# Kernel tuning notes

Measured on AMD Instinct MI355X. Metric: run time of the kernel, lower is better.

## Reference

```python
import jax, jax.numpy as jnp
import numpy as np

N, E, G = 30000, 240000, 1500
EMB, NODE_DIM, EDGE_DIM, TASKS = 300, 9, 3, 12
L_ENC, L_RAT = 5, 2
GAMMA, T_CON = 0.4, 0.2


def _w(key, shape, fan_in):
    return jax.random.normal(key, shape, jnp.float32) / np.float32(np.sqrt(fan_in))


def setup_inputs() -> dict:
    key = jax.random.key(0)
    ks = jax.random.split(key, 32)
    inp = {}
    inp['x'] = jax.random.normal(ks[0], (N, NODE_DIM), jnp.float32)
    inp['edge_attr'] = jax.random.normal(ks[1], (E, EDGE_DIM), jnp.float32)
    inp['edge_index'] = jax.random.randint(ks[2], (2, E), 0, N, jnp.int32)
    b = jnp.sort(jax.random.randint(ks[3], (N,), 0, G, jnp.int32))
    inp['batch'] = b.at[0].set(0).at[-1].set(G - 1)
    u = jax.random.uniform(ks[4], (N, 2), jnp.float32, 1e-6, 1.0 - 1e-6)
    inp['gumbel'] = -jnp.log(-jnp.log(u))  # standard Gumbel noise (tau=1)
    inp['perm'] = jax.random.permutation(ks[5], G).astype(jnp.int32)
    inp['W_enc'] = _w(ks[6], (NODE_DIM, EMB), NODE_DIM)
    inp['b_enc'] = jnp.zeros((EMB,), jnp.float32)
    inp['We_g'] = _w(ks[7], (L_ENC, EDGE_DIM, EMB), EDGE_DIM)
    inp['be_g'] = jnp.zeros((L_ENC, EMB), jnp.float32)
    inp['W1_g'] = _w(ks[8], (L_ENC, EMB, 2 * EMB), EMB)
    inp['b1_g'] = jnp.zeros((L_ENC, 2 * EMB), jnp.float32)
    inp['W2_g'] = _w(ks[9], (L_ENC, 2 * EMB, EMB), 2 * EMB)
    inp['b2_g'] = jnp.zeros((L_ENC, EMB), jnp.float32)
    inp['We_r'] = _w(ks[10], (L_RAT, EDGE_DIM, EMB), EDGE_DIM)
    inp['be_r'] = jnp.zeros((L_RAT, EMB), jnp.float32)
    inp['W1_r'] = _w(ks[11], (L_RAT, EMB, 2 * EMB), EMB)
    inp['b1_r'] = jnp.zeros((L_RAT, 2 * EMB), jnp.float32)
    inp['W2_r'] = _w(ks[12], (L_RAT, 2 * EMB, EMB), 2 * EMB)
    inp['b2_r'] = jnp.zeros((L_RAT, EMB), jnp.float32)
    inp['Wg1'] = _w(ks[13], (EMB, 2 * EMB), EMB)
    inp['bg1'] = jnp.zeros((2 * EMB,), jnp.float32)
    inp['Wg2'] = _w(ks[14], (2 * EMB, 2), 2 * EMB)
    inp['bg2'] = jnp.zeros((2,), jnp.float32)
    inp['Wp1'] = _w(ks[15], (EMB, 2 * EMB), EMB)
    inp['bp1'] = jnp.zeros((2 * EMB,), jnp.float32)
    inp['Wp2'] = _w(ks[16], (2 * EMB, TASKS), 2 * EMB)
    inp['bp2'] = jnp.zeros((TASKS,), jnp.float32)
    return inp


def _gin_stack(x, src, dst, edge_attr, We, be, W1, b1, W2, b2):
    # GIN-style message passing with edge features, residual, JK='last'.
    L = We.shape[0]
    for l in range(L):
        e = edge_attr @ We[l] + be[l]                               # [E, EMB]
        msg = jax.nn.relu(x[src] + e)                                # gather [E, EMB]
        agg = jax.ops.segment_sum(msg, dst, num_segments=x.shape[0])  # scatter [N, EMB]
        h = jax.nn.relu((agg + x) @ W1[l] + b1[l]) @ W2[l] + b2[l]
        if l < L - 1:
            h = jax.nn.relu(h)
        x = x + h  # residual
    return x


def _mlp2(h, Wa, ba, Wb, bb):
    # Linear -> (BN=identity in eval) -> ReLU -> (Dropout=identity) -> Linear
    return jax.nn.relu(h @ Wa + ba) @ Wb + bb


def _forward(x, edge_attr, gumbel, W_enc, b_enc, We_g, be_g, W1_g, b1_g, W2_g, b2_g,
             We_r, be_r, W1_r, b1_r, W2_r, b2_r, Wg1, bg1, Wg2, bg2, Wp1, bp1, Wp2, bp2,
             edge_index, batch, perm):
    src, dst = edge_index[0], edge_index[1]
    cnt = jnp.clip(jax.ops.segment_sum(jnp.ones((x.shape[0],), jnp.float32), batch, num_segments=G), 1.0)[:, None]

    def gmean(v):
        return jax.ops.segment_sum(v, batch, num_segments=G) / cnt

    x_feat = x @ W_enc + b_enc                                      # node encoder
    h_node = _gin_stack(x_feat, src, dst, edge_attr, We_g, be_g, W1_g, b1_g, W2_g, b2_g)
    x_rat = _gin_stack(x_feat, src, dst, edge_attr, We_r, be_r, W1_r, b1_r, W2_r, b2_r)

    gate_logits = _mlp2(x_rat, Wg1, bg1, Wg2, bg2)                  # [N, 2]
    gate = jax.nn.softmax(gate_logits + gumbel, axis=-1)[:, 1:2]     # gumbel-softmax (soft), keep last col

    h_r = gmean(gate * h_node)
    h_env = gmean((1.0 - gate) * h_node)
    r_num = jax.ops.segment_sum(gate, batch, num_segments=G) + 1e-8
    env_num = jax.ops.segment_sum(1.0 - gate, batch, num_segments=G) + 1e-8

    pred_rem = _mlp2(h_r, Wp1, bp1, Wp2, bp2)
    loss_reg = jnp.abs(r_num / (r_num + env_num) - GAMMA).mean()

    h_out = gmean(h_node)
    na = jnp.linalg.norm(h_r, axis=1)
    nb = jnp.linalg.norm(h_out, axis=1)
    nc = jnp.linalg.norm(h_env, axis=1)
    sim = jnp.exp((h_r @ h_out.T) / (na[:, None] * nb[None, :] + 1e-8) / T_CON)
    sim_cp = jnp.exp((h_r @ h_env.T) / (na[:, None] * nc[None, :] + 1e-8) / T_CON)
    pos = jnp.diagonal(sim)
    loss_con = -jnp.log(pos / (sim_cp.sum(axis=1) + pos)).mean()

    pred_rep = _mlp2(h_r + h_env[perm], Wp1, bp1, Wp2, bp2)
    return pred_rep, pred_rem, loss_reg, loss_con


def reference(x, edge_attr, gumbel, W_enc, b_enc, We_g, be_g, W1_g, b1_g, W2_g, b2_g,
              We_r, be_r, W1_r, b1_r, W2_r, b2_r, Wg1, bg1, Wg2, bg2, Wp1, bp1, Wp2, bp2,
              edge_index, batch, perm):
    return _forward(x, edge_attr, gumbel, W_enc, b_enc, We_g, be_g, W1_g, b1_g, W2_g, b2_g,
                    We_r, be_r, W1_r, b1_r, W2_r, b2_r, Wg1, bg1, Wg2, bg2, Wp1, bp1, Wp2, bp2,
                    edge_index, batch, perm)
```

## Files before the change

### kernel.cpp

```cpp
#include <hip/hip_runtime.h>
#include <hip/hip_bf16.h>

typedef __hip_bfloat16 bf16;
typedef __attribute__((ext_vector_type(8))) short bf16x8;
typedef __attribute__((ext_vector_type(4))) float f32x4;

#define NN 30000
#define NE 240000
#define NG 1500
#define EMB 300
#define HID 600
#define NTASK 12
#define SEM 320
#define SHID 608
#define CG 75
#define NBLK_SCAN 118

__device__ __forceinline__ float tof(bf16 v){ return __bfloat162float(v); }
__device__ __forceinline__ bf16  tob(float v){ return __float2bfloat16(v); }
__device__ __forceinline__ float b2f(unsigned short u){ return __uint_as_float(((unsigned)u)<<16); }

__global__ __launch_bounds__(256) void k_zero_i(int* __restrict__ p, int n){
    int i = blockIdx.x*256 + threadIdx.x;
    if (i < n) p[i] = 0;
// ... 40 lines not shown
    for (int off=1; off<256; off<<=1){
        int add = (t>=off) ? s[t-off] : 0;
        __syncthreads();
        s[t] += add;
        __syncthreads();
    }
    int excl = s[t] - v + boff[b];
    if (i < NN){ indptr[i] = excl; cursor[i] = excl; }
    if (i == 0) indptr[NN] = NE;
}

__global__ __launch_bounds__(256) void k_scatter(const int* __restrict__ dst, int* __restrict__ cursor,
                                                 int* __restrict__ eid){
    int e = blockIdx.x*256 + threadIdx.x;
    if (e < NE){ int p = atomicAdd(&cursor[dst[e]], 1); eid[p] = e; }
}

__global__ __launch_bounds__(256) void k_eprep(const int* __restrict__ eid, const int* __restrict__ src,
                                               const float* __restrict__ eattr, float4* __restrict__ epack){
    int k = blockIdx.x*256 + threadIdx.x;
    if (k >= NE) return;
    int e = eid[k];
    float4 p;
    p.x = __int_as_float(src[e]);
    p.y = eattr[e*3]; p.z = eattr[e*3+1]; p.w = eattr[e*3+2];
    epack[k] = p;
}

__global__ __launch_bounds__(256) void k_gstart(const int* __restrict__ batch, int* __restrict__ gstart){
    int g = blockIdx.x*256 + threadIdx.x;
    if (g > NG) return;
    if (g == NG){ gstart[NG] = NN; return; }
    int lo=0, hi=NN;
    while (lo<hi){ int mid=(lo+hi)>>1; if (batch[mid] < g) lo=mid+1; else hi=mid; }
    gstart[g] = lo;
}

__global__ __launch_bounds__(256) void k_wprep(const float* __restrict__ W, bf16* __restrict__ Wt,
                                               int K, int Kp, int N){
    __shared__ float t[32][33];
    const float* Wz = W + (size_t)blockIdx.z*K*N;
    bf16* Wtz = Wt + (size_t)blockIdx.z*N*Kp;
    int n0 = blockIdx.x*32, k0 = blockIdx.y*32;
    int tx = threadIdx.x & 31, ty = threadIdx.x >> 5;
    #pragma unroll
    for (int i=0;i<4;i++){
        int k = k0 + ty + i*8, n = n0 + tx;
        t[ty+i*8][tx] = (k<K && n<N) ? Wz[(size_t)k*N+n] : 0.f;
    }
    __syncthreads();
    #pragma unroll
    for (int i=0;i<4;i++){
        int n = n0 + ty + i*8, k = k0 + tx;
        if (n<N && k<Kp) Wtz[(size_t)n*Kp+k] = tob(t[tx][ty+i*8]);
    }
}

__global__ __launch_bounds__(256) void k_encoder(const float* __restrict__ x, const float* __restrict__ W,
                                                 const float* __restrict__ b, bf16* __restrict__ xfeat){
    int idx = blockIdx.x*256 + threadIdx.x;
    if (idx >= NN*EMB) return;
    int n = idx / EMB, c = idx - n*EMB;
    float acc = b[c];
    #pragma unroll
    for (int k=0;k<9;k++) acc += x[n*9+k] * W[k*EMB+c];
    xfeat[(size_t)n*SEM + c] = tob(acc);
}

__global__ __launch_bounds__(256) void k_agg4(const bf16* __restrict__ cur, const float* __restrict__ We,
                      const float* __restrict__ be, const float4* __restrict__ epack,
                      const int* __restrict__ indptr, bf16* __restrict__ apx){
    int idx = blockIdx.x*256 + threadIdx.x;
    if (idx >= NN*CG) return;
    int n = idx / CG, cg = idx - n*CG;
    int c0 = cg*4;
    float w0[4], w1[4], w2[4], bbv[4], acc[4];
    #pragma unroll
    for (int j=0;j<4;j++){
        w0[j] = We[c0+j]; w1[j] = We[EMB+c0+j]; w2[j] = We[2*EMB+c0+j]; bbv[j] = be[c0+j];
    }
    ushort4 hs = *(const ushort4*)&cur[(size_t)n*SEM + c0];
    acc[0]=b2f(hs.x); acc[1]=b2f(hs.y); acc[2]=b2f(hs.z); acc[3]=b2f(hs.w);
    int k  = indptr[n], k1 = indptr[n+1];
    for (; k+4 <= k1; k += 4){
        float4 e0 = epack[k], e1 = epack[k+1], e2 = epack[k+2], e3 = epack[k+3];
        int s0 = __float_as_int(e0.x), s1 = __float_as_int(e1.x);
        int s2 = __float_as_int(e2.x), s3 = __float_as_int(e3.x);
        ushort4 ha = *(const ushort4*)&cur[(size_t)s0*SEM + c0];
        ushort4 hb = *(const ushort4*)&cur[(size_t)s1*SEM + c0];
        ushort4 hc = *(const ushort4*)&cur[(size_t)s2*SEM + c0];
        ushort4 hd = *(const ushort4*)&cur[(size_t)s3*SEM + c0];
        float fa[4] = {b2f(ha.x), b2f(ha.y), b2f(ha.z), b2f(ha.w)};
        float fb[4] = {b2f(hb.x), b2f(hb.y), b2f(hb.z), b2f(hb.w)};
        float fc[4] = {b2f(hc.x), b2f(hc.y), b2f(hc.z), b2f(hc.w)};
        float fd[4] = {b2f(hd.x), b2f(hd.y), b2f(hd.z), b2f(hd.w)};
        #pragma unroll
        for (int j=0;j<4;j++){
            float va = fa[j] + e0.y*w0[j] + e0.z*w1[j] + e0.w*w2[j] + bbv[j];
            float vb = fb[j] + e1.y*w0[j] + e1.z*w1[j] + e1.w*w2[j] + bbv[j];
            float vc = fc[j] + e2.y*w0[j] + e2.z*w1[j] + e2.w*w2[j] + bbv[j];
            float vd = fd[j] + e3.y*w0[j] + e3.z*w1[j] + e3.w*w2[j] + bbv[j];
            acc[j] += fmaxf(va, 0.f) + fmaxf(vb, 0.f) + fmaxf(vc, 0.f) + fmaxf(vd, 0.f);
        }
    }
    for (; k+2 <= k1; k += 2){
        float4 e0 = epack[k], e1 = epack[k+1];
        int s0 = __float_as_int(e0.x), s1 = __float_as_int(e1.x);
        ushort4 ha = *(const ushort4*)&cur[(size_t)s0*SEM + c0];
        ushort4 hb = *(const ushort4*)&cur[(size_t)s1*SEM + c0];
        float fa[4] = {b2f(ha.x), b2f(ha.y), b2f(ha.z), b2f(ha.w)};
        float fb[4] = {b2f(hb.x), b2f(hb.y), b2f(hb.z), b2f(hb.w)};
        #pragma unroll
        for (int j=0;j<4;j++){
            float va = fa[j] + e0.y*w0[j] + e0.z*w1[j] + e0.w*w2[j] + bbv[j];
            float vb = fb[j] + e1.y*w0[j] + e1.z*w1[j] + e1.w*w2[j] + bbv[j];
            acc[j] += fmaxf(va, 0.f) + fmaxf(vb, 0.f);
        }
    }
    if (k < k1){
        float4 e0 = epack[k];
        int s0 = __float_as_int(e0.x);
        ushort4 ha = *(const ushort4*)&cur[(size_t)s0*SEM + c0];
        float fa[4] = {b2f(ha.x), b2f(ha.y), b2f(ha.z), b2f(ha.w)};
        #pragma unroll
        for (int j=0;j<4;j++){
            float va = fa[j] + e0.y*w0[j] + e0.z*w1[j] + e0.w*w2[j] + bbv[j];
            acc[j] += fmaxf(va, 0.f);
        }
    }
    ushort4 o;
    o.x = __bfloat16_as_ushort(tob(acc[0]));
    o.y = __bfloat16_as_ushort(tob(acc[1]));
    o.z = __bfloat16_as_ushort(tob(acc[2]));
    o.w = __bfloat16_as_ushort(tob(acc[3]));
    *(ushort4*)&apx[(size_t)n*SEM + c0] = o;
}

__global__ __launch_bounds__(256) void k_gemm2(const bf16* __restrict__ A, const bf16* __restrict__ Bt,
        const float* __restrict__ bias, const bf16* __restrict__ R, bf16* __restrict__ C,
        int M, int N, int Kp, int ldc, int relu_out){
    __shared__ __align__(16) char ldsbuf[34816];
    short (*Asl)[64][8] = reinterpret_cast<short(*)[64][8]>(ldsbuf);
    short (*Bsl)[64][8] = reinterpret_cast<short(*)[64][8]>(ldsbuf + 8192);
    short* Ct = reinterpret_cast<short*>(ldsbuf);
    const int CS = 136;
    int tid = threadIdx.x;
    int wave = tid >> 6, lane = tid & 63;
    int wm = wave >> 1, wn = wave & 1;
    int m0 = blockIdx.y*128, n0 = blockIdx.x*128;

    int srow = tid >> 1;
    int sq   = (tid & 1) * 2;
    int grA = min(m0 + srow, M-1);
    int grB = min(n0 + srow, N-1);
    const bf16* pA = A  + (size_t)grA*Kp + sq*8;
    const bf16* pB = Bt + (size_t)grB*Kp + sq*8;
    short* ldsA0 = &Asl[srow>>4][ sq   *16 + (srow&15)][0];
    short* ldsA1 = &Asl[srow>>4][(sq+1)*16 + (srow&15)][0];
    short* ldsB0 = &Bsl[srow>>4][ sq   *16 + (srow&15)][0];
    short* ldsB1 = &Bsl[srow>>4][(sq+1)*16 + (srow&15)][0];

    f32x4 acc[4][4];
    #pragma unroll
    for (int i=0;i<4;i++){
        #pragma unroll
        for (int j=0;j<4;j++) acc[i][j] = (f32x4){0.f,0.f,0.f,0.f};
    }

    int KC = Kp >> 5;
    uint4 ra0 = *(const uint4*)(pA);
    uint4 ra1 = *(const uint4*)(pA + 8);
    uint4 rb0 = *(const uint4*)(pB);
    uint4 rb1 = *(const uint4*)(pB + 8);

    for (int kc=0; kc<KC; ++kc){
        *(uint4*)ldsA0 = ra0; *(uint4*)ldsA1 = ra1;
        *(uint4*)ldsB0 = rb0; *(uint4*)ldsB1 = rb1;
        __syncthreads();
        if (kc+1 < KC){
            const bf16* qA = pA + (kc+1)*32;
            const bf16* qB = pB + (kc+1)*32;
            ra0 = *(const uint4*)(qA); ra1 = *(const uint4*)(qA+8);
            rb0 = *(const uint4*)(qB); rb1 = *(const uint4*)(qB+8);
        }
        bf16x8 af[4], bfr[4];
        #pragma unroll
        for (int i=0;i<4;i++) af[i]  = *(const bf16x8*)&Asl[wm*4+i][lane][0];
        #pragma unroll
        for (int j=0;j<4;j++) bfr[j] = *(const bf16x8*)&Bsl[wn*4+j][lane][0];
        #pragma unroll
        for (int i=0;i<4;i++){
            #pragma unroll
            for (int j=0;j<4;j++)
                acc[i][j] = __builtin_amdgcn_mfma_f32_16x16x32_bf16(af[i], bfr[j], acc[i][j], 0, 0, 0);
        }
        __syncthreads();
    }

    int lq = lane >> 4, lr = lane & 15;
    #pragma unroll
    for (int i=0;i<4;i++){
        int rl = (wm*4+i)*16 + lq*4;
        #pragma unroll
        for (int j=0;j<4;j++){
            int cl = (wn*4+j)*16 + lr;
            float bv = bias[min(n0+cl, N-1)];
            #pragma unroll
            for (int r=0;r<4;r++){
                float v = acc[i][j][r] + bv;
                if (relu_out) v = fmaxf(v, 0.f);
                Ct[(rl+r)*CS + cl] = (short)__bfloat16_as_ushort(tob(v));
            }
        }
    }
    __syncthreads();
    #pragma unroll
    for (int p=0;p<8;p++){
        int rl = p*16 + (tid>>4);
        int cl = (tid&15)*8;
        int row = m0 + rl, col = n0 + cl;
        if (row < M && col < N){
            union { short s8[8]; uint4 v; } u;
            u.v = *(uint4*)&Ct[rl*CS + cl];
            if (R){
                const bf16* rp = &R[(size_t)row*ldc + col];
                #pragma unroll
                for (int e=0;e<8;e++){
                    float v = b2f((unsigned short)u.s8[e]) + tof(rp[e]);
                    u.s8[e] = (short)__bfloat16_as_ushort(tob(v));
                }
            }
            *(uint4*)&C[(size_t)row*ldc + col] = u.v;
        }
    }
}

__device__ __forceinline__ void stage_tile(const short* __restrict__ P, int RB, int K, int r0, int k0,
                                           short (*lds)[64][8], int tid){
    #pragma unroll
    for (int s=0;s<2;s++){
        int seg = tid*2+s;
        int row = seg>>2, q = seg&3;
        int gr = r0 + row;
        int gk = k0 + q*8;
        union { short s8[8]; uint4 v; } u;
        if (gr < RB && gk + 8 <= K){
            const uint2* p = (const uint2*)(P + (size_t)gr*K + gk);
            uint2 lo = p[0], hi = p[1];
            u.v.x = lo.x; u.v.y = lo.y; u.v.z = hi.x; u.v.w = hi.y;
        } else {
            #pragma unroll
            for (int j=0;j<8;j++){
                int kk = gk + j;
                u.s8[j] = (gr < RB && kk < K) ? P[(size_t)gr*K + kk] : (short)0;
            }
        }
        *(uint4*)&lds[row>>4][q*16 + (row&15)][0] = u.v;
    }
}

__global__ __launch_bounds__(256) void k_sim_mfma(const bf16* __restrict__ A, const bf16* __restrict__ Bt,
                      const float* __restrict__ na, const float* __restrict__ nc, float* __restrict__ C){
    __shared__ __align__(16) short Asl[8][64][8];
    __shared__ __align__(16) short Bsl[8][64][8];
    int tid = threadIdx.x;
    int wave = tid >> 6, lane = tid & 63;
    int wm = wave >> 1, wn = wave & 1;
    int m0 = blockIdx.y*128, n0 = blockIdx.x*128;
    f32x4 acc[4][4];
    #pragma unroll
    for (int i=0;i<4;i++){
        #pragma unroll
        for (int j=0;j<4;j++) acc[i][j] = (f32x4){0.f,0.f,0.f,0.f};
    }
    for (int k0=0; k0<SEM; k0+=32){
        stage_tile((const short*)A,  NG, SEM, m0, k0, Asl, tid);
        stage_tile((const short*)Bt, NG, SEM, n0, k0, Bsl, tid);
        __syncthreads();
        bf16x8 af[4], bfr[4];
        #pragma unroll
        for (int i=0;i<4;i++) af[i]  = *(const bf16x8*)&Asl[wm*4+i][lane][0];
        #pragma unroll
        for (int j=0;j<4;j++) bfr[j] = *(const bf16x8*)&Bsl[wn*4+j][lane][0];
        #pragma unroll
        for (int i=0;i<4;i++){
            #pragma unroll
            for (int j=0;j<4;j++)
                acc[i][j] = __builtin_amdgcn_mfma_f32_16x16x32_bf16(af[i], bfr[j], acc[i][j], 0, 0, 0);
        }
        __syncthreads();
    }
    int lq = lane >> 4, lr = lane & 15;
    #pragma unroll
    for (int i=0;i<4;i++){
        int rb = m0 + (wm*4+i)*16 + lq*4;
        #pragma unroll
        for (int j=0;j<4;j++){
            int col = n0 + (wn*4+j)*16 + lr;
            if (col >= NG) continue;
            float ncj = nc[col];
            #pragma unroll
            for (int r=0;r<4;r++){
                int row = rb + r;
                if (row >= NG) continue;
                C[(size_t)row*NG+col] = expf(acc[i][j][r] * 5.0f / (na[row]*ncj + 1e-8f));
            }
        }
    }
}

__global__ __launch_bounds__(256) void k_gate(const bf16* __restrict__ mid, const float* __restrict__ Wg2,
                      const float* __restrict__ bg2, const float* __restrict__ gumbel, float* __restrict__ gate){
    int gw = blockIdx.x*4 + (threadIdx.x >> 6);
    int lane = threadIdx.x & 63;
    if (gw >= NN) return;
    float s0=0.f, s1=0.f;
// ... 112 lines not shown
    #pragma unroll
    for (int t=0;t<NTASK;t++) acc[t] = 0.f;
    for (int i=lane;i<HID;i+=64){
        float h = tof(hidP[(size_t)r*SHID+i]);
        const float4* wp = (const float4*)&Wp2[i*NTASK];
        float4 wa = wp[0], wb = wp[1], wc = wp[2];
        acc[0]+=h*wa.x; acc[1]+=h*wa.y; acc[2]+=h*wa.z; acc[3]+=h*wa.w;
        acc[4]+=h*wb.x; acc[5]+=h*wb.y; acc[6]+=h*wb.z; acc[7]+=h*wb.w;
        acc[8]+=h*wc.x; acc[9]+=h*wc.y; acc[10]+=h*wc.z; acc[11]+=h*wc.w;
    }
    #pragma unroll
    for (int t=0;t<NTASK;t++){
        for (int off=32; off>0; off>>=1) acc[t] += __shfl_down(acc[t], off);
    }
    if (lane==0){
        float* dst = (r < NG) ? &out[NG*NTASK + r*NTASK] : &out[(r-NG)*NTASK];
        #pragma unroll
        for (int t=0;t<NTASK;t++) dst[t] = acc[t] + bp2[t];
    }
}

__global__ __launch_bounds__(256) void k_loss(const float* __restrict__ cntf, const float* __restrict__ rnum,
                      const float* __restrict__ pos, const float* __restrict__ S, float* __restrict__ out){
    __shared__ float ra[256], rb[256];
    int t = threadIdx.x;
    float a=0.f, b=0.f;
    for (int g=t; g<NG; g+=256){
        float r = rnum[g] + 1e-8f;
        float e = (cntf[g] - rnum[g]) + 1e-8f;
        a += fabsf(r/(r+e) - 0.4f);
        float p = pos[g];
        b += -logf(p/(S[g]+p));
    }
    ra[t]=a; rb[t]=b; __syncthreads();
    for (int off=128; off>0; off>>=1){ if (t<off){ ra[t]+=ra[t+off]; rb[t]+=rb[t+off]; } __syncthreads(); }
    if (t==0){
        out[2*NG*NTASK]   = ra[0]/NG;
        out[2*NG*NTASK+1] = rb[0]/NG;
    }
}

extern "C" void kernel_launch(void* const* d_in, const int* in_sizes, int n_in,
                              void* d_out, int out_size, void* d_ws, size_t ws_size,
                              hipStream_t stream) {
    const float* x      = (const float*)d_in[0];
    const float* eattr  = (const float*)d_in[1];
    const int*   eidx   = (const int*)d_in[2];
    const int*   batch  = (const int*)d_in[3];
    const float* gumbel = (const float*)d_in[4];
    const int*   perm   = (const int*)d_in[5];
    const float* W_enc  = (const float*)d_in[6];
    const float* b_enc  = (const float*)d_in[7];
    const float* We_g   = (const float*)d_in[8];
    const float* be_g   = (const float*)d_in[9];
    const float* W1_g   = (const float*)d_in[10];
    const float* b1_g   = (const float*)d_in[11];
    const float* W2_g   = (const float*)d_in[12];
    const float* b2_g   = (const float*)d_in[13];
    const float* We_r   = (const float*)d_in[14];
    const float* be_r   = (const float*)d_in[15];
    const float* W1_r   = (const float*)d_in[16];
    const float* b1_r   = (const float*)d_in[17];
    const float* W2_r   = (const float*)d_in[18];
    const float* b2_r   = (const float*)d_in[19];
    const float* Wg1    = (const float*)d_in[20];
    const float* bg1    = (const float*)d_in[21];
    const float* Wg2    = (const float*)d_in[22];
    const float* bg2    = (const float*)d_in[23];
    const float* Wp1    = (const float*)d_in[24];
    const float* bp1    = (const float*)d_in[25];
    const float* Wp2    = (const float*)d_in[26];
    const float* bp2    = (const float*)d_in[27];
    float* out = (float*)d_out;

    const int* srcArr = eidx;
    const int* dstArr = eidx + NE;

    char* w = (char*)d_ws;
    size_t off = 0;
    auto alloc = [&](size_t bytes)->char*{ char* p = w + off; off += (bytes + 255) & ~(size_t)255; return p; };
    bf16* xfeat = (bf16*)alloc((size_t)NN*SEM*2);
    bf16* cur   = (bf16*)alloc((size_t)NN*SEM*2);
    bf16* apx   = (bf16*)alloc((size_t)NN*SEM*2);
    char* midc  = alloc((size_t)NN*SHID*2);
    bf16* mid   = (bf16*)midc;
    float* simcp = (float*)midc;
    bf16* Pbuf   = (bf16*)(midc + 12*1024*1024);
    bf16* hidP   = (bf16*)(midc + 20*1024*1024);
    bf16* wt1g  = (bf16*)alloc((size_t)5*HID*SEM*2);
    bf16* wt2g  = (bf16*)alloc((size_t)5*EMB*SHID*2);
    bf16* wt1r  = (bf16*)alloc((size_t)2*HID*SEM*2);
    bf16* wt2r  = (bf16*)alloc((size_t)2*EMB*SHID*2);
    bf16* wtg1  = (bf16*)alloc((size_t)HID*SEM*2);
    bf16* wtp1  = (bf16*)alloc((size_t)HID*SEM*2);
    float4* epack = (float4*)alloc((size_t)NE*16);
    float* gate  = (float*)alloc((size_t)NN*4);
    float* sumh  = (float*)alloc((size_t)NG*EMB*4);
    float* sumgh = (float*)alloc((size_t)NG*EMB*4);
    float* hr    = (float*)alloc((size_t)NG*EMB*4);
    float* henv  = (float*)alloc((size_t)NG*EMB*4);
    float* hout  = (float*)alloc((size_t)NG*EMB*4);
    bf16* hrb    = (bf16*)alloc((size_t)NG*SEM*2);
    bf16* henvb  = (bf16*)alloc((size_t)NG*SEM*2);
    float* rnum  = (float*)alloc(NG*4);
    float* cntf  = (float*)alloc(NG*4);
    float* na    = (float*)alloc(NG*4);
    float* ncv   = (float*)alloc(NG*4);
    float* pos   = (float*)alloc(NG*4);
    float* Ssum  = (float*)alloc(NG*4);
    int* deg     = (int*)alloc((size_t)NN*4);
    int* indptr  = (int*)alloc((size_t)(NN+1)*4);
    int* cursor  = (int*)alloc((size_t)NN*4);
    int* eid     = (int*)alloc((size_t)NE*4);
    int* gstart  = (int*)alloc((size_t)(NG+1)*4);
    int* bsum    = (int*)alloc((size_t)NBLK_SCAN*4);
    int* boff    = (int*)alloc((size_t)NBLK_SCAN*4);

    const int NB_NE  = (NE+255)/256;
    const int NB_NC  = (NN*EMB+255)/256;
    const int NB_AG  = (NN*CG+255)/256;
    const int NB_GP  = (NG*SEM+255)/256;

    k_zero_i <<<(NN+255)/256, 256, 0, stream>>>(deg, NN);
    k_hist   <<<NB_NE, 256, 0, stream>>>(dstArr, deg);
    k_scanA  <<<NBLK_SCAN, 256, 0, stream>>>(deg, bsum);
    k_scanB  <<<1, 128, 0, stream>>>(bsum, boff);
    k_scanC  <<<NBLK_SCAN, 256, 0, stream>>>(deg, boff, indptr, cursor);
    k_scatter<<<NB_NE, 256, 0, stream>>>(dstArr, cursor, eid);
    k_eprep  <<<NB_NE, 256, 0, stream>>>(eid, srcArr, eattr, epack);
    k_gstart <<<(NG+256)/256, 256, 0, stream>>>(batch, gstart);

    {
        dim3 g1t((HID+31)/32, SEM/32, 5);
        dim3 g2t((EMB+31)/32, SHID/32, 5);
        k_wprep<<<g1t, 256, 0, stream>>>(W1_g, wt1g, EMB, SEM, HID);
        k_wprep<<<g2t, 256, 0, stream>>>(W2_g, wt2g, HID, SHID, EMB);
        dim3 g1t2((HID+31)/32, SEM/32, 2);
        dim3 g2t2((EMB+31)/32, SHID/32, 2);
        k_wprep<<<g1t2, 256, 0, stream>>>(W1_r, wt1r, EMB, SEM, HID);
        k_wprep<<<g2t2, 256, 0, stream>>>(W2_r, wt2r, HID, SHID, EMB);
        dim3 g1t1((HID+31)/32, SEM/32, 1);
        k_wprep<<<g1t1, 256, 0, stream>>>(Wg1, wtg1, EMB, SEM, HID);
        k_wprep<<<g1t1, 256, 0, stream>>>(Wp1, wtp1, EMB, SEM, HID);
    }

    dim3 gm1((HID+127)/128, (NN+127)/128);
    dim3 gm2((EMB+127)/128, (NN+127)/128);

    k_encoder<<<NB_NC, 256, 0, stream>>>(x, W_enc, b_enc, xfeat);

    for (int l=0; l<2; l++){
        const bf16* in = (l==0) ? xfeat : cur;
        k_agg4 <<<NB_AG, 256, 0, stream>>>(in, We_r + l*3*EMB, be_r + l*EMB, epack, indptr, apx);
        k_gemm2<<<gm1, 256, 0, stream>>>(apx, wt1r + (size_t)l*HID*SEM, b1_r + l*HID, nullptr, mid,
                                         NN, HID, SEM, SHID, 1);
        k_gemm2<<<gm2, 256, 0, stream>>>(mid, wt2r + (size_t)l*EMB*SHID, b2_r + l*EMB, in, cur,
                                         NN, EMB, SHID, SEM, (l<1)?1:0);
    }
    k_gemm2<<<gm1, 256, 0, stream>>>(cur, wtg1, bg1, nullptr, mid, NN, HID, SEM, SHID, 1);
    k_gate<<<NN/4, 256, 0, stream>>>(mid, Wg2, bg2, gumbel, gate);

    for (int l=0; l<5; l++){
        const bf16* in = (l==0) ? xfeat : cur;
        k_agg4 <<<NB_AG, 256, 0, stream>>>(in, We_g + l*3*EMB, be_g + l*EMB, epack, indptr, apx);
        k_gemm2<<<gm1, 256, 0, stream>>>(apx, wt1g + (size_t)l*HID*SEM, b1_g + l*HID, nullptr, mid,
                                         NN, HID, SEM, SHID, 1);
        k_gemm2<<<gm2, 256, 0, stream>>>(mid, wt2g + (size_t)l*EMB*SHID, b2_g + l*EMB, in, cur,
                                         NN, EMB, SHID, SEM, (l<4)?1:0);
    }

    k_pool  <<<NG, 320, 0, stream>>>(cur, gate, gstart, sumh, sumgh);
    k_rnum  <<<(NG+3)/4, 256, 0, stream>>>(gate, gstart, rnum, cntf);
    k_mean  <<<NB_GP, 256, 0, stream>>>(sumh, sumgh, cntf, hr, henv, hout, hrb, henvb);
    k_pbuild<<<NB_GP, 256, 0, stream>>>(hr, henv, perm, Pbuf);
    k_norm  <<<(NG+3)/4, 256, 0, stream>>>(hr, henv, hout, na, ncv, pos);
    dim3 gsim((NG+127)/128, (NG+127)/128);
    k_sim_mfma<<<gsim, 256, 0, stream>>>(hrb, henvb, na, ncv, simcp);
    k_rowsum<<<NG, 256, 0, stream>>>(simcp, Ssum);
    dim3 gph((HID+127)/128, (2*NG+127)/128);
    k_gemm2<<<gph, 256, 0, stream>>>(Pbuf, wtp1, bp1, nullptr, hidP, 2*NG, HID, SEM, SHID, 1);
    k_pred  <<<(2*NG+3)/4, 256, 0, stream>>>(hidP, Wp2, bp2, out);
    k_loss  <<<1, 256, 0, stream>>>(cntf, rnum, pos, Ssum, out);
}
```

Before: 996.6 us.

## Widen GEMM tiles to 128x256 and software-pipeline gather loads in aggregation

```diff
diff --git a/kernel.cpp b/kernel.cpp
--- a/kernel.cpp
+++ b/kernel.cpp
@@ -146,14 +146,9 @@
     ushort4 hs = *(const ushort4*)&cur[(size_t)n*SEM + c0];
     acc[0]=b2f(hs.x); acc[1]=b2f(hs.y); acc[2]=b2f(hs.z); acc[3]=b2f(hs.w);
     int k  = indptr[n], k1 = indptr[n+1];
-    for (; k+4 <= k1; k += 4){
-        float4 e0 = epack[k], e1 = epack[k+1], e2 = epack[k+2], e3 = epack[k+3];
-        int s0 = __float_as_int(e0.x), s1 = __float_as_int(e1.x);
-        int s2 = __float_as_int(e2.x), s3 = __float_as_int(e3.x);
-        ushort4 ha = *(const ushort4*)&cur[(size_t)s0*SEM + c0];
-        ushort4 hb = *(const ushort4*)&cur[(size_t)s1*SEM + c0];
-        ushort4 hc = *(const ushort4*)&cur[(size_t)s2*SEM + c0];
-        ushort4 hd = *(const ushort4*)&cur[(size_t)s3*SEM + c0];
+
+    auto accum4 = [&](float4 e0, float4 e1, float4 e2, float4 e3,
+                      ushort4 ha, ushort4 hb, ushort4 hc, ushort4 hd){
         float fa[4] = {b2f(ha.x), b2f(ha.y), b2f(ha.z), b2f(ha.w)};
         float fb[4] = {b2f(hb.x), b2f(hb.y), b2f(hb.z), b2f(hb.w)};
         float fc[4] = {b2f(hc.x), b2f(hc.y), b2f(hc.z), b2f(hc.w)};
@@ -166,22 +161,29 @@
             float vd = fd[j] + e3.y*w0[j] + e3.z*w1[j] + e3.w*w2[j] + bbv[j];
             acc[j] += fmaxf(va, 0.f) + fmaxf(vb, 0.f) + fmaxf(vc, 0.f) + fmaxf(vd, 0.f);
         }
-    }
-    for (; k+2 <= k1; k += 2){
-        float4 e0 = epack[k], e1 = epack[k+1];
-        int s0 = __float_as_int(e0.x), s1 = __float_as_int(e1.x);
-        ushort4 ha = *(const ushort4*)&cur[(size_t)s0*SEM + c0];
-        ushort4 hb = *(const ushort4*)&cur[(size_t)s1*SEM + c0];
-        float fa[4] = {b2f(ha.x), b2f(ha.y), b2f(ha.z), b2f(ha.w)};
-        float fb[4] = {b2f(hb.x), b2f(hb.y), b2f(hb.z), b2f(hb.w)};
-        #pragma unroll
-        for (int j=0;j<4;j++){
-            float va = fa[j] + e0.y*w0[j] + e0.z*w1[j] + e0.w*w2[j] + bbv[j];
-            float vb = fb[j] + e1.y*w0[j] + e1.z*w1[j] + e1.w*w2[j] + bbv[j];
-            acc[j] += fmaxf(va, 0.f) + fmaxf(vb, 0.f);
-        }
-    }
-    if (k < k1){
+    };
+
+    if (k + 4 <= k1){
+        float4 e0 = epack[k], e1 = epack[k+1], e2 = epack[k+2], e3 = epack[k+3];
+        ushort4 h0 = *(const ushort4*)&cur[(size_t)__float_as_int(e0.x)*SEM + c0];
+        ushort4 h1 = *(const ushort4*)&cur[(size_t)__float_as_int(e1.x)*SEM + c0];
+        ushort4 h2 = *(const ushort4*)&cur[(size_t)__float_as_int(e2.x)*SEM + c0];
+        ushort4 h3 = *(const ushort4*)&cur[(size_t)__float_as_int(e3.x)*SEM + c0];
+        while (k + 8 <= k1){
+            float4 f0 = epack[k+4], f1 = epack[k+5], f2 = epack[k+6], f3 = epack[k+7];
+            ushort4 g0 = *(const ushort4*)&cur[(size_t)__float_as_int(f0.x)*SEM + c0];
+            ushort4 g1 = *(const ushort4*)&cur[(size_t)__float_as_int(f1.x)*SEM + c0];
+            ushort4 g2 = *(const ushort4*)&cur[(size_t)__float_as_int(f2.x)*SEM + c0];
+            ushort4 g3 = *(const ushort4*)&cur[(size_t)__float_as_int(f3.x)*SEM + c0];
+            accum4(e0,e1,e2,e3, h0,h1,h2,h3);
+            e0=f0; e1=f1; e2=f2; e3=f3;
+            h0=g0; h1=g1; h2=g2; h3=g3;
+            k += 4;
+        }
+        accum4(e0,e1,e2,e3, h0,h1,h2,h3);
+        k += 4;
+    }
+    for (; k < k1; k++){
         float4 e0 = epack[k];
         int s0 = __float_as_int(e0.x);
         ushort4 ha = *(const ushort4*)&cur[(size_t)s0*SEM + c0];
@@ -200,9 +202,13 @@
     *(ushort4*)&apx[(size_t)n*SEM + c0] = o;
 }
 
-__global__ __launch_bounds__(256) void k_gemm2(const bf16* __restrict__ A, const bf16* __restrict__ Bt,
+template<int NF>
+__global__ __launch_bounds__(256) void k_gemmT(const bf16* __restrict__ A, const bf16* __restrict__ Bt,
         const float* __restrict__ bias, const bf16* __restrict__ R, bf16* __restrict__ C,
         int M, int N, int Kp, int ldc, int relu_out){
+    constexpr int TN = NF*32;
+    constexpr int SB = (TN*4)/256;
+    constexpr int PASSES = NF/4;
     __shared__ __align__(16) char ldsbuf[34816];
     short (*Asl)[64][8] = reinterpret_cast<short(*)[64][8]>(ldsbuf);
     short (*Bsl)[64][8] = reinterpret_cast<short(*)[64][8]>(ldsbuf + 8192);
@@ -211,51 +217,56 @@
     int tid = threadIdx.x;
     int wave = tid >> 6, lane = tid & 63;
     int wm = wave >> 1, wn = wave & 1;
-    int m0 = blockIdx.y*128, n0 = blockIdx.x*128;
-
-    int srow = tid >> 1;
-    int sq   = (tid & 1) * 2;
-    int grA = min(m0 + srow, M-1);
-    int grB = min(n0 + srow, N-1);
-    const bf16* pA = A  + (size_t)grA*Kp + sq*8;
-    const bf16* pB = Bt + (size_t)grB*Kp + sq*8;
-    short* ldsA0 = &Asl[srow>>4][ sq   *16 + (srow&15)][0];
-    short* ldsA1 = &Asl[srow>>4][(sq+1)*16 + (srow&15)][0];
-    short* ldsB0 = &Bsl[srow>>4][ sq   *16 + (srow&15)][0];
-    short* ldsB1 = &Bsl[srow>>4][(sq+1)*16 + (srow&15)][0];
-
-    f32x4 acc[4][4];
+    int m0 = blockIdx.y*128, n0 = blockIdx.x*TN;
+
+    int arow = tid >> 1, aq = (tid & 1)*2;
+    int grA = min(m0 + arow, M-1);
+    const bf16* pA = A + (size_t)grA*Kp + aq*8;
+    short* ldsA0 = &Asl[arow>>4][ aq   *16 + (arow&15)][0];
+    short* ldsA1 = &Asl[arow>>4][(aq+1)*16 + (arow&15)][0];
+    const bf16* pB[SB]; short* ldsB[SB];
+    #pragma unroll
+    for (int s=0;s<SB;s++){
+        int g = tid*SB + s; int br = g >> 2, bq = g & 3;
+        int grB = min(n0 + br, N-1);
+        pB[s] = Bt + (size_t)grB*Kp + bq*8;
+        ldsB[s] = &Bsl[br>>4][bq*16 + (br&15)][0];
+    }
+
+    f32x4 acc[4][NF];
     #pragma unroll
     for (int i=0;i<4;i++){
         #pragma unroll
-        for (int j=0;j<4;j++) acc[i][j] = (f32x4){0.f,0.f,0.f,0.f};
+        for (int j=0;j<NF;j++) acc[i][j] = (f32x4){0.f,0.f,0.f,0.f};
     }
 
     int KC = Kp >> 5;
-    uint4 ra0 = *(const uint4*)(pA);
+    uint4 ra0 = *(const uint4*)pA;
     uint4 ra1 = *(const uint4*)(pA + 8);
-    uint4 rb0 = *(const uint4*)(pB);
-    uint4 rb1 = *(const uint4*)(pB + 8);
+    uint4 rb[SB];
+    #pragma unroll
+    for (int s=0;s<SB;s++) rb[s] = *(const uint4*)pB[s];
 
     for (int kc=0; kc<KC; ++kc){
         *(uint4*)ldsA0 = ra0; *(uint4*)ldsA1 = ra1;
-        *(uint4*)ldsB0 = rb0; *(uint4*)ldsB1 = rb1;
+        #pragma unroll
+        for (int s=0;s<SB;s++) *(uint4*)ldsB[s] = rb[s];
         __syncthreads();
         if (kc+1 < KC){
             const bf16* qA = pA + (kc+1)*32;
-            const bf16* qB = pB + (kc+1)*32;
             ra0 = *(const uint4*)(qA); ra1 = *(const uint4*)(qA+8);
-            rb0 = *(const uint4*)(qB); rb1 = *(const uint4*)(qB+8);
-        }
-        bf16x8 af[4], bfr[4];
+            #pragma unroll
+            for (int s=0;s<SB;s++) rb[s] = *(const uint4*)(pB[s] + (kc+1)*32);
+        }
+        bf16x8 af[4], bfr[NF];
         #pragma unroll
         for (int i=0;i<4;i++) af[i]  = *(const bf16x8*)&Asl[wm*4+i][lane][0];
         #pragma unroll
-        for (int j=0;j<4;j++) bfr[j] = *(const bf16x8*)&Bsl[wn*4+j][lane][0];
+        for (int j=0;j<NF;j++) bfr[j] = *(const bf16x8*)&Bsl[wn*NF+j][lane][0];
         #pragma unroll
         for (int i=0;i<4;i++){
             #pragma unroll
-            for (int j=0;j<4;j++)
+            for (int j=0;j<NF;j++)
                 acc[i][j] = __builtin_amdgcn_mfma_f32_16x16x32_bf16(af[i], bfr[j], acc[i][j], 0, 0, 0);
         }
         __syncthreads();
@@ -263,39 +274,47 @@
 
     int lq = lane >> 4, lr = lane & 15;
     #pragma unroll
-    for (int i=0;i<4;i++){
-        int rl = (wm*4+i)*16 + lq*4;
-        #pragma unroll
-        for (int j=0;j<4;j++){
-            int cl = (wn*4+j)*16 + lr;
-            float bv = bias[min(n0+cl, N-1)];
+    for (int h=0; h<PASSES; h++){
+        if (PASSES == 1 || wn == h){
             #pragma unroll
-            for (int r=0;r<4;r++){
-                float v = acc[i][j][r] + bv;
-                if (relu_out) v = fmaxf(v, 0.f);
-                Ct[(rl+r)*CS + cl] = (short)__bfloat16_as_ushort(tob(v));
-            }
-        }
-    }
-    __syncthreads();
-    #pragma unroll
-    for (int p=0;p<8;p++){
-        int rl = p*16 + (tid>>4);
-        int cl = (tid&15)*8;
-        int row = m0 + rl, col = n0 + cl;
-        if (row < M && col < N){
-            union { short s8[8]; uint4 v; } u;
-            u.v = *(uint4*)&Ct[rl*CS + cl];
-            if (R){
-                const bf16* rp = &R[(size_t)row*ldc + col];
+            for (int i=0;i<4;i++){
+                int rl = (wm*4+i)*16 + lq*4;
                 #pragma unroll
-                for (int e=0;e<8;e++){
-                    float v = b2f((unsigned short)u.s8[e]) + tof(rp[e]);
-                    u.s8[e] = (short)__bfloat16_as_ushort(tob(v));
+                for (int j=0;j<NF;j++){
+                    int fl = (PASSES==1) ? (wn*4+j) : j;
+                    int cl = fl*16 + lr;
+                    int gcol = n0 + h*128 + cl;
+                    float bv = bias[min(gcol, N-1)];
+                    #pragma unroll
+                    for (int r=0;r<4;r++){
+                        float v = acc[i][j][r] + bv;
+                        if (relu_out) v = fmaxf(v, 0.f);
+                        Ct[(rl+r)*CS + cl] = (short)__bfloat16_as_ushort(tob(v));
+                    }
                 }
             }
-            *(uint4*)&C[(size_t)row*ldc + col] = u.v;
-        }
+        }
+        __syncthreads();
+        #pragma unroll
+        for (int p=0;p<8;p++){
+            int rl = p*16 + (tid>>4);
+            int cl = (tid&15)*8;
+            int row = m0 + rl, col = n0 + h*128 + cl;
+            if (row < M && col < N){
+                union { short s8[8]; uint4 v; } u;
+                u.v = *(uint4*)&Ct[rl*CS + cl];
+                if (R){
+                    const bf16* rp = &R[(size_t)row*ldc + col];
+                    #pragma unroll
+                    for (int e=0;e<8;e++){
+                        float v = b2f((unsigned short)u.s8[e]) + tof(rp[e]);
+                        u.s8[e] = (short)__bfloat16_as_ushort(tob(v));
+                    }
+                }
+                *(uint4*)&C[(size_t)row*ldc + col] = u.v;
+            }
+        }
+        if (h+1 < PASSES) __syncthreads();
     }
 }
 
@@ -636,29 +655,29 @@
         k_wprep<<<g1t1, 256, 0, stream>>>(Wp1, wtp1, EMB, SEM, HID);
     }
 
-    dim3 gm1((HID+127)/128, (NN+127)/128);
-    dim3 gm2((EMB+127)/128, (NN+127)/128);
+    dim3 gm1((HID+255)/256, (NN+127)/128);
+    dim3 gm2((EMB+255)/256, (NN+127)/128);
 
     k_encoder<<<NB_NC, 256, 0, stream>>>(x, W_enc, b_enc, xfeat);
 
     for (int l=0; l<2; l++){
         const bf16* in = (l==0) ? xfeat : cur;
         k_agg4 <<<NB_AG, 256, 0, stream>>>(in, We_r + l*3*EMB, be_r + l*EMB, epack, indptr, apx);
-        k_gemm2<<<gm1, 256, 0, stream>>>(apx, wt1r + (size_t)l*HID*SEM, b1_r + l*HID, nullptr, mid,
-                                         NN, HID, SEM, SHID, 1);
-        k_gemm2<<<gm2, 256, 0, stream>>>(mid, wt2r + (size_t)l*EMB*SHID, b2_r + l*EMB, in, cur,
-                                         NN, EMB, SHID, SEM, (l<1)?1:0);
-    }
-    k_gemm2<<<gm1, 256, 0, stream>>>(cur, wtg1, bg1, nullptr, mid, NN, HID, SEM, SHID, 1);
+        k_gemmT<8><<<gm1, 256, 0, stream>>>(apx, wt1r + (size_t)l*HID*SEM, b1_r + l*HID, nullptr, mid,
+                                            NN, HID, SEM, SHID, 1);
+        k_gemmT<8><<<gm2, 256, 0, stream>>>(mid, wt2r + (size_t)l*EMB*SHID, b2_r + l*EMB, in, cur,
+                                            NN, EMB, SHID, SEM, (l<1)?1:0);
+    }
+    k_gemmT<8><<<gm1, 256, 0, stream>>>(cur, wtg1, bg1, nullptr, mid, NN, HID, SEM, SHID, 1);
     k_gate<<<NN/4, 256, 0, stream>>>(mid, Wg2, bg2, gumbel, gate);
 
     for (int l=0; l<5; l++){
         const bf16* in = (l==0) ? xfeat : cur;
         k_agg4 <<<NB_AG, 256, 0, stream>>>(in, We_g + l*3*EMB, be_g + l*EMB, epack, indptr, apx);
-        k_gemm2<<<gm1, 256, 0, stream>>>(apx, wt1g + (size_t)l*HID*SEM, b1_g + l*HID, nullptr, mid,
-                                         NN, HID, SEM, SHID, 1);
-        k_gemm2<<<gm2, 256, 0, stream>>>(mid, wt2g + (size_t)l*EMB*SHID, b2_g + l*EMB, in, cur,
-                                         NN, EMB, SHID, SEM, (l<4)?1:0);
+        k_gemmT<8><<<gm1, 256, 0, stream>>>(apx, wt1g + (size_t)l*HID*SEM, b1_g + l*HID, nullptr, mid,
+                                            NN, HID, SEM, SHID, 1);
+        k_gemmT<8><<<gm2, 256, 0, stream>>>(mid, wt2g + (size_t)l*EMB*SHID, b2_g + l*EMB, in, cur,
+                                            NN, EMB, SHID, SEM, (l<4)?1:0);
     }
 
     k_pool  <<<NG, 320, 0, stream>>>(cur, gate, gstart, sumh, sumgh);
@@ -669,8 +688,8 @@
     dim3 gsim((NG+127)/128, (NG+127)/128);
     k_sim_mfma<<<gsim, 256, 0, stream>>>(hrb, henvb, na, ncv, simcp);
     k_rowsum<<<NG, 256, 0, stream>>>(simcp, Ssum);
-    dim3 gph((HID+127)/128, (2*NG+127)/128);
-    k_gemm2<<<gph, 256, 0, stream>>>(Pbuf, wtp1, bp1, nullptr, hidP, 2*NG, HID, SEM, SHID, 1);
+    dim3 gph((HID+255)/256, (2*NG+127)/128);
+    k_gemmT<8><<<gph, 256, 0, stream>>>(Pbuf, wtp1, bp1, nullptr, hidP, 2*NG, HID, SEM, SHID, 1);
     k_pred  <<<(2*NG+3)/4, 256, 0, stream>>>(hidP, Wp2, bp2, out);
     k_loss  <<<1, 256, 0, stream>>>(cntf, rnum, pos, Ssum, out);
 }
```

Result: slower. 1.749 ms (+75.5%).

## Fuse first-layer aggregations of both GIN stacks, prefetch gathers, halve GEMM LDS

Applied to the files above, without the earlier changes.

```diff
diff --git a/kernel.cpp b/kernel.cpp
--- a/kernel.cpp
+++ b/kernel.cpp
@@ -146,14 +146,9 @@
     ushort4 hs = *(const ushort4*)&cur[(size_t)n*SEM + c0];
     acc[0]=b2f(hs.x); acc[1]=b2f(hs.y); acc[2]=b2f(hs.z); acc[3]=b2f(hs.w);
     int k  = indptr[n], k1 = indptr[n+1];
-    for (; k+4 <= k1; k += 4){
-        float4 e0 = epack[k], e1 = epack[k+1], e2 = epack[k+2], e3 = epack[k+3];
-        int s0 = __float_as_int(e0.x), s1 = __float_as_int(e1.x);
-        int s2 = __float_as_int(e2.x), s3 = __float_as_int(e3.x);
-        ushort4 ha = *(const ushort4*)&cur[(size_t)s0*SEM + c0];
-        ushort4 hb = *(const ushort4*)&cur[(size_t)s1*SEM + c0];
-        ushort4 hc = *(const ushort4*)&cur[(size_t)s2*SEM + c0];
-        ushort4 hd = *(const ushort4*)&cur[(size_t)s3*SEM + c0];
+
+    auto accum4 = [&](float4 e0, float4 e1, float4 e2, float4 e3,
+                      ushort4 ha, ushort4 hb, ushort4 hc, ushort4 hd){
         float fa[4] = {b2f(ha.x), b2f(ha.y), b2f(ha.z), b2f(ha.w)};
         float fb[4] = {b2f(hb.x), b2f(hb.y), b2f(hb.z), b2f(hb.w)};
         float fc[4] = {b2f(hc.x), b2f(hc.y), b2f(hc.z), b2f(hc.w)};
@@ -166,7 +161,68 @@
             float vd = fd[j] + e3.y*w0[j] + e3.z*w1[j] + e3.w*w2[j] + bbv[j];
             acc[j] += fmaxf(va, 0.f) + fmaxf(vb, 0.f) + fmaxf(vc, 0.f) + fmaxf(vd, 0.f);
         }
-    }
+    };
+
+    if (k + 4 <= k1){
+        float4 e0 = epack[k], e1 = epack[k+1], e2 = epack[k+2], e3 = epack[k+3];
+        ushort4 h0 = *(const ushort4*)&cur[(size_t)__float_as_int(e0.x)*SEM + c0];
+        ushort4 h1 = *(const ushort4*)&cur[(size_t)__float_as_int(e1.x)*SEM + c0];
+        ushort4 h2 = *(const ushort4*)&cur[(size_t)__float_as_int(e2.x)*SEM + c0];
+        ushort4 h3 = *(const ushort4*)&cur[(size_t)__float_as_int(e3.x)*SEM + c0];
+        while (k + 8 <= k1){
+            float4 f0 = epack[k+4], f1 = epack[k+5], f2 = epack[k+6], f3 = epack[k+7];
+            ushort4 g0 = *(const ushort4*)&cur[(size_t)__float_as_int(f0.x)*SEM + c0];
+            ushort4 g1 = *(const ushort4*)&cur[(size_t)__float_as_int(f1.x)*SEM + c0];
+            ushort4 g2 = *(const ushort4*)&cur[(size_t)__float_as_int(f2.x)*SEM + c0];
+            ushort4 g3 = *(const ushort4*)&cur[(size_t)__float_as_int(f3.x)*SEM + c0];
+            accum4(e0,e1,e2,e3, h0,h1,h2,h3);
+            e0=f0; e1=f1; e2=f2; e3=f3;
+            h0=g0; h1=g1; h2=g2; h3=g3;
+            k += 4;
+        }
+        accum4(e0,e1,e2,e3, h0,h1,h2,h3);
+        k += 4;
+    }
+    for (; k < k1; k++){
+        float4 e0 = epack[k];
+        int s0 = __float_as_int(e0.x);
+        ushort4 ha = *(const ushort4*)&cur[(size_t)s0*SEM + c0];
+        float fa[4] = {b2f(ha.x), b2f(ha.y), b2f(ha.z), b2f(ha.w)};
+        #pragma unroll
+        for (int j=0;j<4;j++){
+            float va = fa[j] + e0.y*w0[j] + e0.z*w1[j] + e0.w*w2[j] + bbv[j];
+            acc[j] += fmaxf(va, 0.f);
+        }
+    }
+    ushort4 o;
+    o.x = __bfloat16_as_ushort(tob(acc[0]));
+    o.y = __bfloat16_as_ushort(tob(acc[1]));
+    o.z = __bfloat16_as_ushort(tob(acc[2]));
+    o.w = __bfloat16_as_ushort(tob(acc[3]));
+    *(ushort4*)&apx[(size_t)n*SEM + c0] = o;
+}
+
+__global__ __launch_bounds__(256) void k_agg4d(const bf16* __restrict__ cur,
+                      const float* __restrict__ WeA, const float* __restrict__ beA,
+                      const float* __restrict__ WeB, const float* __restrict__ beB,
+                      const float4* __restrict__ epack, const int* __restrict__ indptr,
+                      bf16* __restrict__ apxA, bf16* __restrict__ apxB){
+    int idx = blockIdx.x*256 + threadIdx.x;
+    if (idx >= NN*CG) return;
+    int n = idx / CG, cg = idx - n*CG;
+    int c0 = cg*4;
+    float a0[4], a1[4], a2[4], ab[4], accA[4];
+    float b0[4], b1[4], b2[4], bb[4], accB[4];
+    #pragma unroll
+    for (int j=0;j<4;j++){
+        a0[j]=WeA[c0+j]; a1[j]=WeA[EMB+c0+j]; a2[j]=WeA[2*EMB+c0+j]; ab[j]=beA[c0+j];
+        b0[j]=WeB[c0+j]; b1[j]=WeB[EMB+c0+j]; b2[j]=WeB[2*EMB+c0+j]; bb[j]=beB[c0+j];
+    }
+    ushort4 hs = *(const ushort4*)&cur[(size_t)n*SEM + c0];
+    float fs[4] = {b2f(hs.x), b2f(hs.y), b2f(hs.z), b2f(hs.w)};
+    #pragma unroll
+    for (int j=0;j<4;j++){ accA[j]=fs[j]; accB[j]=fs[j]; }
+    int k = indptr[n], k1 = indptr[n+1];
     for (; k+2 <= k1; k += 2){
         float4 e0 = epack[k], e1 = epack[k+1];
         int s0 = __float_as_int(e0.x), s1 = __float_as_int(e1.x);
@@ -176,9 +232,10 @@
         float fb[4] = {b2f(hb.x), b2f(hb.y), b2f(hb.z), b2f(hb.w)};
         #pragma unroll
         for (int j=0;j<4;j++){
-            float va = fa[j] + e0.y*w0[j] + e0.z*w1[j] + e0.w*w2[j] + bbv[j];
-            float vb = fb[j] + e1.y*w0[j] + e1.z*w1[j] + e1.w*w2[j] + bbv[j];
-            acc[j] += fmaxf(va, 0.f) + fmaxf(vb, 0.f);
+            accA[j] += fmaxf(fa[j] + e0.y*a0[j] + e0.z*a1[j] + e0.w*a2[j] + ab[j], 0.f)
+                     + fmaxf(fb[j] + e1.y*a0[j] + e1.z*a1[j] + e1.w*a2[j] + ab[j], 0.f);
+            accB[j] += fmaxf(fa[j] + e0.y*b0[j] + e0.z*b1[j] + e0.w*b2[j] + bb[j], 0.f)
+                     + fmaxf(fb[j] + e1.y*b0[j] + e1.z*b1[j] + e1.w*b2[j] + bb[j], 0.f);
         }
     }
     if (k < k1){
@@ -188,22 +245,23 @@
         float fa[4] = {b2f(ha.x), b2f(ha.y), b2f(ha.z), b2f(ha.w)};
         #pragma unroll
         for (int j=0;j<4;j++){
-            float va = fa[j] + e0.y*w0[j] + e0.z*w1[j] + e0.w*w2[j] + bbv[j];
-            acc[j] += fmaxf(va, 0.f);
-        }
-    }
-    ushort4 o;
-    o.x = __bfloat16_as_ushort(tob(acc[0]));
-    o.y = __bfloat16_as_ushort(tob(acc[1]));
-    o.z = __bfloat16_as_ushort(tob(acc[2]));
-    o.w = __bfloat16_as_ushort(tob(acc[3]));
-    *(ushort4*)&apx[(size_t)n*SEM + c0] = o;
+            accA[j] += fmaxf(fa[j] + e0.y*a0[j] + e0.z*a1[j] + e0.w*a2[j] + ab[j], 0.f);
+            accB[j] += fmaxf(fa[j] + e0.y*b0[j] + e0.z*b1[j] + e0.w*b2[j] + bb[j], 0.f);
+        }
+    }
+    ushort4 oA, oB;
+    oA.x=__bfloat16_as_ushort(tob(accA[0])); oA.y=__bfloat16_as_ushort(tob(accA[1]));
+    oA.z=__bfloat16_as_ushort(tob(accA[2])); oA.w=__bfloat16_as_ushort(tob(accA[3]));
+    oB.x=__bfloat16_as_ushort(tob(accB[0])); oB.y=__bfloat16_as_ushort(tob(accB[1]));
+    oB.z=__bfloat16_as_ushort(tob(accB[2])); oB.w=__bfloat16_as_ushort(tob(accB[3]));
+    *(ushort4*)&apxA[(size_t)n*SEM + c0] = oA;
+    *(ushort4*)&apxB[(size_t)n*SEM + c0] = oB;
 }
 
 __global__ __launch_bounds__(256) void k_gemm2(const bf16* __restrict__ A, const bf16* __restrict__ Bt,
         const float* __restrict__ bias, const bf16* __restrict__ R, bf16* __restrict__ C,
         int M, int N, int Kp, int ldc, int relu_out){
-    __shared__ __align__(16) char ldsbuf[34816];
+    __shared__ __align__(16) char ldsbuf[17408];
     short (*Asl)[64][8] = reinterpret_cast<short(*)[64][8]>(ldsbuf);
     short (*Bsl)[64][8] = reinterpret_cast<short(*)[64][8]>(ldsbuf + 8192);
     short* Ct = reinterpret_cast<short*>(ldsbuf);
@@ -263,39 +321,45 @@
 
     int lq = lane >> 4, lr = lane & 15;
     #pragma unroll
-    for (int i=0;i<4;i++){
-        int rl = (wm*4+i)*16 + lq*4;
-        #pragma unroll
-        for (int j=0;j<4;j++){
-            int cl = (wn*4+j)*16 + lr;
-            float bv = bias[min(n0+cl, N-1)];
+    for (int h=0; h<2; h++){
+        if (wm == h){
             #pragma unroll
-            for (int r=0;r<4;r++){
-                float v = acc[i][j][r] + bv;
-                if (relu_out) v = fmaxf(v, 0.f);
-                Ct[(rl+r)*CS + cl] = (short)__bfloat16_as_ushort(tob(v));
-            }
-        }
-    }
-    __syncthreads();
-    #pragma unroll
-    for (int p=0;p<8;p++){
-        int rl = p*16 + (tid>>4);
-        int cl = (tid&15)*8;
-        int row = m0 + rl, col = n0 + cl;
-        if (row < M && col < N){
-            union { short s8[8]; uint4 v; } u;
-            u.v = *(uint4*)&Ct[rl*CS + cl];
-            if (R){
-                const bf16* rp = &R[(size_t)row*ldc + col];
+            for (int i=0;i<4;i++){
+                int rl = i*16 + lq*4;
                 #pragma unroll
-                for (int e=0;e<8;e++){
-                    float v = b2f((unsigned short)u.s8[e]) + tof(rp[e]);
-                    u.s8[e] = (short)__bfloat16_as_ushort(tob(v));
+                for (int j=0;j<4;j++){
+                    int cl = (wn*4+j)*16 + lr;
+                    float bv = bias[min(n0+cl, N-1)];
+                    #pragma unroll
+                    for (int r=0;r<4;r++){
+                        float v = acc[i][j][r] + bv;
+                        if (relu_out) v = fmaxf(v, 0.f);
+                        Ct[(rl+r)*CS + cl] = (short)__bfloat16_as_ushort(tob(v));
+                    }
                 }
             }
-            *(uint4*)&C[(size_t)row*ldc + col] = u.v;
-        }
+        }
+        __syncthreads();
+        #pragma unroll
+        for (int p=0;p<4;p++){
+            int rl = p*16 + (tid>>4);
+            int cl = (tid&15)*8;
+            int row = m0 + h*64 + rl, col = n0 + cl;
+            if (row < M && col < N){
+                union { short s8[8]; uint4 v; } u;
+                u.v = *(uint4*)&Ct[rl*CS + cl];
+                if (R){
+                    const bf16* rp = &R[(size_t)row*ldc + col];
+                    #pragma unroll
+                    for (int e=0;e<8;e++){
+                        float v = b2f((unsigned short)u.s8[e]) + tof(rp[e]);
+                        u.s8[e] = (short)__bfloat16_as_ushort(tob(v));
+                    }
+                }
+                *(uint4*)&C[(size_t)row*ldc + col] = u.v;
+            }
+        }
+        if (h == 0) __syncthreads();
     }
 }
 
@@ -574,6 +638,7 @@
     bf16* xfeat = (bf16*)alloc((size_t)NN*SEM*2);
     bf16* cur   = (bf16*)alloc((size_t)NN*SEM*2);
     bf16* apx   = (bf16*)alloc((size_t)NN*SEM*2);
+    bf16* apx2  = (bf16*)alloc((size_t)NN*SEM*2);
     char* midc  = alloc((size_t)NN*SHID*2);
     bf16* mid   = (bf16*)midc;
     float* simcp = (float*)midc;
@@ -641,9 +706,12 @@
 
     k_encoder<<<NB_NC, 256, 0, stream>>>(x, W_enc, b_enc, xfeat);
 
+    k_agg4d<<<NB_AG, 256, 0, stream>>>(xfeat, We_r, be_r, We_g, be_g, epack, indptr, apx, apx2);
+
     for (int l=0; l<2; l++){
         const bf16* in = (l==0) ? xfeat : cur;
-        k_agg4 <<<NB_AG, 256, 0, stream>>>(in, We_r + l*3*EMB, be_r + l*EMB, epack, indptr, apx);
+        if (l > 0)
+            k_agg4 <<<NB_AG, 256, 0, stream>>>(in, We_r + l*3*EMB, be_r + l*EMB, epack, indptr, apx);
         k_gemm2<<<gm1, 256, 0, stream>>>(apx, wt1r + (size_t)l*HID*SEM, b1_r + l*HID, nullptr, mid,
                                          NN, HID, SEM, SHID, 1);
         k_gemm2<<<gm2, 256, 0, stream>>>(mid, wt2r + (size_t)l*EMB*SHID, b2_r + l*EMB, in, cur,
@@ -654,8 +722,10 @@
 
     for (int l=0; l<5; l++){
         const bf16* in = (l==0) ? xfeat : cur;
-        k_agg4 <<<NB_AG, 256, 0, stream>>>(in, We_g + l*3*EMB, be_g + l*EMB, epack, indptr, apx);
-        k_gemm2<<<gm1, 256, 0, stream>>>(apx, wt1g + (size_t)l*HID*SEM, b1_g + l*HID, nullptr, mid,
+        const bf16* ap = (l==0) ? apx2 : apx;
+        if (l > 0)
+            k_agg4 <<<NB_AG, 256, 0, stream>>>(in, We_g + l*3*EMB, be_g + l*EMB, epack, indptr, apx);
+        k_gemm2<<<gm1, 256, 0, stream>>>(ap, wt1g + (size_t)l*HID*SEM, b1_g + l*HID, nullptr, mid,
                                          NN, HID, SEM, SHID, 1);
         k_gemm2<<<gm2, 256, 0, stream>>>(mid, wt2g + (size_t)l*EMB*SHID, b2_g + l*EMB, in, cur,
                                          NN, EMB, SHID, SEM, (l<4)?1:0);
```

New measurement: 1.038 ms. 1.04x slower.
